# Kernel optimization log

Measured on AMD Instinct MI355X. Metric: run time of the kernel, lower is better.

The kernel has to match this reference:

```python
import jax, jax.numpy as jnp
import numpy as np

KERNEL = 301  # sliding max window length (odd -> same-size output)
TOPK = 2


def setup_inputs() -> dict:
    key = jax.random.key(0)
    xcorr = jax.random.normal(key, (32, 3, 64, 8192), dtype=jnp.float32)
    return {"xcorr": xcorr, "nlag": 4096}


def reference(xcorr, nlag):
    # xcorr: [nb, nc, nx, nt]
    x = jnp.abs(xcorr)  # vabs=True
    pad = KERNEL // 2
    # sliding-window max over time axis (== F.max_pool2d((1,K), stride 1, pad K//2))
    smax = jax.lax.reduce_window(
        x,
        -jnp.inf,
        jax.lax.max,
        window_dimensions=(1, 1, 1, KERNEL),
        window_strides=(1, 1, 1, 1),
        padding=[(0, 0), (0, 0), (0, 0), (pad, pad)],
    )
    # keep only local maxima, zero elsewhere (x * (smax == x).float())
    scores = jnp.where(smax == x, x, jnp.zeros((), x.dtype))
    topk_score, topk_idx = jax.lax.top_k(scores, TOPK)  # [nb, nc, nx, TOPK]
    return topk_score, topk_idx
```

## Files before the change

### kernel.cpp

```cpp
#include <hip/hip_runtime.h>
#include <stdint.h>


#define NT 8192
#define RADIUS 150
#define NSEG 256

__global__ __launch_bounds__(256) void detect_peaks_kernel(
    const float* __restrict__ x, float* __restrict__ out, int nrows)
{
    const int row = blockIdx.x;
    const int s = threadIdx.x;

    __shared__ float mm[8 + NSEG + 16];
    __shared__ unsigned long long wred[8];
    float* const mmp = mm + 8;

    const float4* g4 = (const float4*)(x + (size_t)row * NT);

    if (s < 8) mm[s] = 0.0f;
    if (s < 16) mm[8 + NSEG + s] = 0.0f;

    float4 vv[8];
#pragma unroll
    for (int j = 0; j < 8; ++j) vv[j] = g4[s * 8 + j];

    float sval = 0.0f;
#pragma unroll
    for (int j = 0; j < 8; ++j) {
        float4 v = vv[j];
        v.x = fabsf(v.x); v.y = fabsf(v.y);
        v.z = fabsf(v.z); v.w = fabsf(v.w);
        vv[j] = v;
        sval = fmaxf(sval, fmaxf(fmaxf(v.x, v.y), fmaxf(v.z, v.w)));
    }
    mmp[s] = sval;
    __syncthreads();

    float nbr[9];
#pragma unroll
    for (int j = 0; j < 9; ++j) nbr[j] = mmp[s - 4 + j];
    float nb7 = 0.0f;
#pragma unroll
    for (int j = 1; j <= 7; ++j) nb7 = fmaxf(nb7, nbr[j]);

    unsigned long long k1 = 0ull, k2 = 0ull;

    if (!(nb7 > sval)) {
        unsigned eqm = 0u;
#pragma unroll
        for (int j = 0; j < 8; ++j) {
            eqm |= (vv[j].x == sval ? 1u : 0u) << (4 * j + 0);
            eqm |= (vv[j].y == sval ? 1u : 0u) << (4 * j + 1);
            eqm |= (vv[j].z == sval ? 1u : 0u) << (4 * j + 2);
            eqm |= (vv[j].w == sval ? 1u : 0u) << (4 * j + 3);
        }
        while (eqm) {
            const int b = __builtin_ctz(eqm); eqm &= (eqm - 1u);
            const int t = (s << 5) + b;
            const int l = max(t - RADIUS, 0);
            const int r = min(t + RADIUS, NT - 1);
            const int il = l >> 5, ir = r >> 5;
            float im = 0.0f;
#pragma unroll
            for (int j = 0; j < 9; ++j) {
                const int seg = s - 4 + j;
                im = fmaxf(im, (seg >= il + 1 && seg <= ir - 1) ? nbr[j] : 0.0f);
            }
            if (im > sval) continue;
            float em = 0.0f;
            {
                const int hb0 = l >> 2;
                const int hbN = il * 8 + 8;
#pragma unroll
                for (int j = 0; j < 8; ++j) {
                    const int bb = hb0 + j;
                    const float4 q = g4[bb];
                    float bm;
                    if (j == 0) {
                        bm = (4 * bb + 0 >= l) ? fabsf(q.x) : 0.0f;
                        bm = fmaxf(bm, (4 * bb + 1 >= l) ? fabsf(q.y) : 0.0f);
                        bm = fmaxf(bm, (4 * bb + 2 >= l) ? fabsf(q.z) : 0.0f);
                        bm = fmaxf(bm, fabsf(q.w));
                    } else {
                        bm = fmaxf(fmaxf(fabsf(q.x), fabsf(q.y)),
                                   fmaxf(fabsf(q.z), fabsf(q.w)));
                    }
                    em = fmaxf(em, (bb < hbN) ? bm : 0.0f);
                }
            }
            {
                const int tb0 = ir * 8;
#pragma unroll
                for (int j = 0; j < 8; ++j) {
                    const int bb = tb0 + j;
                    const float4 q = g4[bb];
                    float bm;
                    bm = (4 * bb + 0 <= r) ? fabsf(q.x) : 0.0f;
                    bm = fmaxf(bm, (4 * bb + 1 <= r) ? fabsf(q.y) : 0.0f);
                    bm = fmaxf(bm, (4 * bb + 2 <= r) ? fabsf(q.z) : 0.0f);
                    bm = fmaxf(bm, (4 * bb + 3 <= r) ? fabsf(q.w) : 0.0f);
                    em = fmaxf(em, bm);
                }
            }
            if (em > sval) continue;
            const unsigned long long key =
                ((unsigned long long)__float_as_uint(sval) << 32) |
                (unsigned)(NT - 1 - t);
            if (key > k1) { k2 = k1; k1 = key; }
            else if (key > k2) { k2 = key; }
        }
    }

#pragma unroll
    for (int off = 32; off >= 1; off >>= 1) {
        unsigned long long o1 = __shfl_down(k1, off);
        unsigned long long o2 = __shfl_down(k2, off);
        unsigned long long hi = (k1 > o1) ? k1 : o1;
        unsigned long long lo = (k1 > o1) ? o1 : k1;
        unsigned long long s2 = (k2 > o2) ? k2 : o2;
        k1 = hi;
        k2 = (lo > s2) ? lo : s2;
    }
    const int wave = s >> 6;
    if ((s & 63) == 0) { wred[wave * 2] = k1; wred[wave * 2 + 1] = k2; }
    __syncthreads();

    if (s == 0) {
        unsigned long long a1 = wred[0], a2 = wred[1];
        for (int wv = 1; wv < 4; ++wv) {
            unsigned long long o1 = wred[wv * 2], o2 = wred[wv * 2 + 1];
            unsigned long long hi = (a1 > o1) ? a1 : o1;
            unsigned long long lo = (a1 > o1) ? o1 : a1;
            unsigned long long s2 = (a2 > o2) ? a2 : o2;
            a1 = hi;
            a2 = (lo > s2) ? lo : s2;
        }
        float s1v, s2v; int i1, i2;
        if (a1 == 0ull) { s1v = 0.0f; i1 = 0; }
        else {
            s1v = __uint_as_float((unsigned)(a1 >> 32));
            i1 = (NT - 1) - (int)(a1 & 0xffffffffull);
        }
        if (a2 == 0ull) {
            s2v = 0.0f;
            i2 = (i1 == 0) ? 1 : 0;
        } else {
            s2v = __uint_as_float((unsigned)(a2 >> 32));
            i2 = (NT - 1) - (int)(a2 & 0xffffffffull);
        }
        out[row * 2 + 0] = s1v;
        out[row * 2 + 1] = s2v;
        float* oi = out + (size_t)nrows * 2;
        oi[row * 2 + 0] = (float)i1;
        oi[row * 2 + 1] = (float)i2;
    }
}

extern "C" void kernel_launch(void* const* d_in, const int* in_sizes, int n_in,
                              void* d_out, int out_size, void* d_ws, size_t ws_size,
                              hipStream_t stream) {
    const float* x = (const float*)d_in[0];
    float* out = (float*)d_out;
    const int nrows = in_sizes[0] / NT;
    detect_peaks_kernel<<<nrows, 256, 0, stream>>>(x, out, nrows);
}
```

Baseline: 273.7 us.

## Stage row in swizzled LDS with coalesced nontemporal loads; read edges from LDS

Each block now loads its row with fully coalesced nontemporal float4 loads (stride 256 per iteration instead of a per-thread contiguous 128-byte chunk). It stores the absolute values into an XOR-swizzled 32KB LDS buffer and re-reads the per-thread contiguous chunk from LDS. The edge-block checks for peak candidates read from LDS instead of re-issuing global loads. The cost is 32KB of LDS per block, which can reduce occupancy, plus an extra barrier and an LDS round trip.

```diff
diff --git a/kernel.cpp b/kernel.cpp
--- a/kernel.cpp
+++ b/kernel.cpp
@@ -5,6 +5,9 @@
 #define NT 8192
 #define RADIUS 150
 #define NSEG 256
+#define NF4 2048
+
+typedef float f4 __attribute__((ext_vector_type(4)));
 
 __global__ __launch_bounds__(256) void detect_peaks_kernel(
     const float* __restrict__ x, float* __restrict__ out, int nrows)
@@ -12,26 +15,39 @@
     const int row = blockIdx.x;
     const int s = threadIdx.x;
 
+    __shared__ f4 lds4[NF4];
     __shared__ float mm[8 + NSEG + 16];
     __shared__ unsigned long long wred[8];
     float* const mmp = mm + 8;
 
-    const float4* g4 = (const float4*)(x + (size_t)row * NT);
+    const f4* g4 = (const f4*)(x + (size_t)row * NT);
 
     if (s < 8) mm[s] = 0.0f;
     if (s < 16) mm[8 + NSEG + s] = 0.0f;
 
-    float4 vv[8];
+    f4 ld[8];
 #pragma unroll
-    for (int j = 0; j < 8; ++j) vv[j] = g4[s * 8 + j];
+    for (int j = 0; j < 8; ++j)
+        ld[j] = __builtin_nontemporal_load(g4 + j * 256 + s);
+    const int wsw = (s >> 3) & 7;
+#pragma unroll
+    for (int j = 0; j < 8; ++j) {
+        f4 v = ld[j];
+        v.x = fabsf(v.x); v.y = fabsf(v.y);
+        v.z = fabsf(v.z); v.w = fabsf(v.w);
+        lds4[(j * 256 + s) ^ wsw] = v;
+    }
+    __syncthreads();
+
+    f4 vv[8];
+    const int rsw = s & 7;
+#pragma unroll
+    for (int j = 0; j < 8; ++j) vv[j] = lds4[(s * 8 + j) ^ rsw];
 
     float sval = 0.0f;
 #pragma unroll
     for (int j = 0; j < 8; ++j) {
-        float4 v = vv[j];
-        v.x = fabsf(v.x); v.y = fabsf(v.y);
-        v.z = fabsf(v.z); v.w = fabsf(v.w);
-        vv[j] = v;
+        f4 v = vv[j];
         sval = fmaxf(sval, fmaxf(fmaxf(v.x, v.y), fmaxf(v.z, v.w)));
     }
     mmp[s] = sval;
@@ -75,16 +91,15 @@
 #pragma unroll
                 for (int j = 0; j < 8; ++j) {
                     const int bb = hb0 + j;
-                    const float4 q = g4[bb];
+                    const f4 q = lds4[bb ^ ((bb >> 3) & 7)];
                     float bm;
                     if (j == 0) {
-                        bm = (4 * bb + 0 >= l) ? fabsf(q.x) : 0.0f;
-                        bm = fmaxf(bm, (4 * bb + 1 >= l) ? fabsf(q.y) : 0.0f);
-                        bm = fmaxf(bm, (4 * bb + 2 >= l) ? fabsf(q.z) : 0.0f);
-                        bm = fmaxf(bm, fabsf(q.w));
+                        bm = (4 * bb + 0 >= l) ? q.x : 0.0f;
+                        bm = fmaxf(bm, (4 * bb + 1 >= l) ? q.y : 0.0f);
+                        bm = fmaxf(bm, (4 * bb + 2 >= l) ? q.z : 0.0f);
+                        bm = fmaxf(bm, q.w);
                     } else {
-                        bm = fmaxf(fmaxf(fabsf(q.x), fabsf(q.y)),
-                                   fmaxf(fabsf(q.z), fabsf(q.w)));
+                        bm = fmaxf(fmaxf(q.x, q.y), fmaxf(q.z, q.w));
                     }
                     em = fmaxf(em, (bb < hbN) ? bm : 0.0f);
                 }
@@ -94,12 +109,12 @@
 #pragma unroll
                 for (int j = 0; j < 8; ++j) {
                     const int bb = tb0 + j;
-                    const float4 q = g4[bb];
+                    const f4 q = lds4[bb ^ ((bb >> 3) & 7)];
                     float bm;
-                    bm = (4 * bb + 0 <= r) ? fabsf(q.x) : 0.0f;
-                    bm = fmaxf(bm, (4 * bb + 1 <= r) ? fabsf(q.y) : 0.0f);
-                    bm = fmaxf(bm, (4 * bb + 2 <= r) ? fabsf(q.z) : 0.0f);
-                    bm = fmaxf(bm, (4 * bb + 3 <= r) ? fabsf(q.w) : 0.0f);
+                    bm = (4 * bb + 0 <= r) ? q.x : 0.0f;
+                    bm = fmaxf(bm, (4 * bb + 1 <= r) ? q.y : 0.0f);
+                    bm = fmaxf(bm, (4 * bb + 2 <= r) ? q.z : 0.0f);
+                    bm = fmaxf(bm, (4 * bb + 3 <= r) ? q.w : 0.0f);
                     em = fmaxf(em, bm);
                 }
             }
```

Measured after the change: 256.5 us. 6.3% less time.
